# Kernel tuning notes

Measured on AMD Instinct MI355X. Metric: run time of the kernel, lower is better.

The kernel has to match this reference:

```python
import jax, jax.numpy as jnp
import numpy as np

B, N, H, M = 1, 1024, 64, 32


def _posenc(n, d):
    # sinusoidal positional encoding, matches torch PositionalEncoding (eval mode, no dropout)
    pos = jnp.arange(n, dtype=jnp.float32)[:, None]
    div = jnp.exp(jnp.arange(0, d, 2, dtype=jnp.float32) * (-np.log(10000.0) / d))
    ang = pos * div  # [n, d//2]
    pe = jnp.zeros((n, d), jnp.float32)
    pe = pe.at[:, 0::2].set(jnp.sin(ang))
    pe = pe.at[:, 1::2].set(jnp.cos(ang))
    return pe


def _egnn(x, h, m2f, w_msg, b_msg, w_pos, b_pos, w_feat, b_feat):
    # x: [B,N,3], h: [B,N,Hd], m2f: [B,N,N] float pair mask (diag zero)
    Bn, Nn, Hd = h.shape
    m2 = m2f[..., None]
    # r[b,i,j] = x[b,j] - x[b,i]  (torch: x.unsqueeze(-3) - x.unsqueeze(-2))
    r = (x[:, None, :, :] - x[:, :, None, :]) * m2  # [B,N,N,3]
    d2 = jnp.sum(r * r, axis=-1)  # [B,N,N]
    # message_mlp(cat(hi, hj, d2)): hi[b,i,j]=h[j], hj[b,i,j]=h[i]
    # split weight to avoid materializing the N x N x (2H+1) concat
    Wa, Wb, wd = w_msg[:, :Hd], w_msg[:, Hd:2 * Hd], w_msg[:, 2 * Hd]
    A = h @ Wa.T   # [B,N,M], contribution of h_j (hi slot)
    Bm = h @ Wb.T  # [B,N,M], contribution of h_i (hj slot)
    m = jax.nn.relu(A[:, None, :, :] + Bm[:, :, None, :] + d2[..., None] * wd + b_msg) * m2  # [B,N,N,M]
    mx = (m @ w_pos.T + b_pos) * r  # [B,N,N,3]
    x = x + jnp.sum(mx, axis=-2) / (Nn - 1)
    msum = jnp.sum(m, axis=-2)  # [B,N,M]
    h = jnp.concatenate([h, msum], axis=-1) @ w_feat.T + b_feat  # [B,N,Hd]
    return x, h


def setup_inputs() -> dict:
    key = jax.random.key(0)
    ks = jax.random.split(key, 16)
    def lin_w(k, o, i):
        return (jax.random.normal(k, (o, i), jnp.float32) / np.sqrt(i)).astype(jnp.float32)
    def lin_b(k, o):
        return (jax.random.normal(k, (o,), jnp.float32) * 0.02).astype(jnp.float32)
    return {
        'positions': jax.random.normal(ks[0], (B, N, 3), jnp.float32),
        'features': jax.random.normal(ks[1], (B, N, H), jnp.float32),
        'mask': jnp.ones((B, N), dtype=bool),
        'w_msg1': lin_w(ks[2], M, 2 * H + 1), 'b_msg1': lin_b(ks[3], M),
        'w_pos1': lin_w(ks[4], 3, M), 'b_pos1': lin_b(ks[5], 3),
        'w_feat1': lin_w(ks[6], H, M + H), 'b_feat1': lin_b(ks[7], H),
        'w_msg2': lin_w(ks[8], M, 2 * H + 1), 'b_msg2': lin_b(ks[9], M),
        'w_pos2': lin_w(ks[10], 3, M), 'b_pos2': lin_b(ks[11], 3),
        'w_feat2': lin_w(ks[12], H, M + H), 'b_feat2': lin_b(ks[13], H),
        't': 0,
    }


def reference(positions, features, mask,
              w_msg1, b_msg1, w_pos1, b_pos1, w_feat1, b_feat1,
              w_msg2, b_msg2, w_pos2, b_pos2, w_feat2, b_feat2, t):
    Bn, Nn, Hd = features.shape
    h = features + _posenc(Nn, Hd)[None]
    mask2 = mask[:, None, :] & mask[:, :, None]
    mask2 = mask2 & (~jnp.eye(Nn, dtype=bool))[None]  # zero self-pairs
    m2f = mask2.astype(positions.dtype)
    x = positions
    x, h = _egnn(x, h, m2f, w_msg1, b_msg1, w_pos1, b_pos1, w_feat1, b_feat1)
    h = jax.nn.relu(h)
    x, h = _egnn(x, h, m2f, w_msg2, b_msg2, w_pos2, b_pos2, w_feat2, b_feat2)
    return x
```

## Files before the change

kernel.cpp:

```cpp
#include <hip/hip_runtime.h>

#define N    1024
#define HD   64
#define MD   32
#define BLK  256
#define BLKP 512
#define WROW (2 * HD + 1)

__global__ __launch_bounds__(BLK) void k_p0(const float* __restrict__ feat,
                                            const float* __restrict__ wmsg,
                                            const float* __restrict__ bmsg,
                                            float* __restrict__ h0,
                                            float* __restrict__ A,
                                            float* __restrict__ Bb)
{
    __shared__ float scr[4160 + 4 * HD];
    const int tid = threadIdx.x;
    const int n0  = blockIdx.x * 4;

    for (int u = tid; u < MD * WROW; u += BLK) scr[u] = wmsg[u];
    float* hrow = scr + 4160;
    {
        const int n = n0 + (tid >> 6), d = tid & 63;
        const float div = expf((float)(d & ~1) * (-9.210340371976184f / 64.0f));
        const float ang = (float)n * div;
        const float pe  = (d & 1) ? cosf(ang) : sinf(ang);
        const float hv  = feat[n * HD + d] + pe;
        h0[n * HD + d] = hv;
        hrow[tid] = hv;
    }
    __syncthreads();
    if (tid < 4 * MD) {
        const int nl = tid >> 5, m = tid & 31;
        const float* wa = scr + m * WROW;
        const float* hr = hrow + nl * HD;
        float sa = 0.f, sb = bmsg[m];
#pragma unroll
        for (int c = 0; c < HD; c++) {
            const float hv = hr[c];
            sa = fmaf(hv, wa[c], sa);
            sb = fmaf(hv, wa[HD + c], sb);
        }
        const int n = n0 + nl;
        A[n * MD + m]  = sa;
        Bb[n * MD + m] = sb;
    }
}

template<int LAYER1>
__global__ __launch_bounds__(BLKP) void k_pair(
    const float* __restrict__ xsrc, const float* __restrict__ Aap,
    const float* __restrict__ Bbp, const float* __restrict__ wmsg,
    const float* __restrict__ wpos, const float* __restrict__ bpos,
    float* __restrict__ xout,
    const float* __restrict__ h0, const float* __restrict__ wf,
    const float* __restrict__ bf, const float* __restrict__ wmsg2,
    const float* __restrict__ bmsg2, float* __restrict__ A2,
    float* __restrict__ B2)
{
    const int tid   = threadIdx.x;
    const int wid   = tid >> 6;
    const int lane  = tid & 63;
    const int jslot = lane & 7;
    const int kq    = lane >> 3;

    __shared__ float4 rd[2 * N];
    __shared__ float  wacc[8][8];
    __shared__ float  msAl[8][MD];
    __shared__ float  msBl[8][MD];
    __shared__ float  SxL[3];
    __shared__ float  msF[2][MD];
    __shared__ float  h0r[2][HD];
    __shared__ float  h1r[2][HD];
    float4* rdA = rd;
    float4* rdB = rd + N;

    const int iA = blockIdx.x, iB = blockIdx.x + N / 2;
    const float xiA0 = xsrc[iA * 3 + 0], xiA1 = xsrc[iA * 3 + 1], xiA2 = xsrc[iA * 3 + 2];
    const float xiB0 = xsrc[iB * 3 + 0], xiB1 = xsrc[iB * 3 + 1], xiB2 = xsrc[iB * 3 + 2];

    float sx0 = 0.f, sx1 = 0.f, sx2 = 0.f;
#pragma unroll
    for (int q = 0; q < N / BLKP; q++) {
        const int j = q * BLKP + tid;
        const float xj0 = xsrc[j * 3 + 0];
        const float xj1 = xsrc[j * 3 + 1];
        const float xj2 = xsrc[j * 3 + 2];
        sx0 += xj0; sx1 += xj1; sx2 += xj2;
        float r0 = xj0 - xiA0, r1 = xj1 - xiA1, r2 = xj2 - xiA2;
        rdA[j] = make_float4(r0, r1, r2, fmaf(r0, r0, fmaf(r1, r1, r2 * r2)));
        r0 = xj0 - xiB0; r1 = xj1 - xiB1; r2 = xj2 - xiB2;
        rdB[j] = make_float4(r0, r1, r2, fmaf(r0, r0, fmaf(r1, r1, r2 * r2)));
    }
#pragma unroll
    for (int off = 32; off > 0; off >>= 1) {
        sx0 += __shfl_xor(sx0, off);
        sx1 += __shfl_xor(sx1, off);
        sx2 += __shfl_xor(sx2, off);
    }
    if (lane == 0) { wacc[wid][0] = sx0; wacc[wid][1] = sx1; wacc[wid][2] = sx2; }
    __syncthreads();
    if (tid == 0) {
        float s0 = 0.f, s1 = 0.f, s2 = 0.f;
#pragma unroll
        for (int w = 0; w < 8; w++) { s0 += wacc[w][0]; s1 += wacc[w][1]; s2 += wacc[w][2]; }
        SxL[0] = s0; SxL[1] = s1; SxL[2] = s2;
    }

    const float4 biA4 = *(const float4*)(Bbp + iA * MD + kq * 4);
    const float4 biB4 = *(const float4*)(Bbp + iB * MD + kq * 4);
    const float4 wpx4 = *(const float4*)(wpos + kq * 4);
    const float4 wpy4 = *(const float4*)(wpos + MD + kq * 4);
    const float4 wpz4 = *(const float4*)(wpos + 2 * MD + kq * 4);
    float wd4[4];
#pragma unroll
    for (int kk = 0; kk < 4; kk++) wd4[kk] = wmsg[(kq * 4 + kk) * WROW + 2 * HD];
    const float biA[4] = {biA4.x, biA4.y, biA4.z, biA4.w};
    const float biB[4] = {biB4.x, biB4.y, biB4.z, biB4.w};
    const float wpx[4] = {wpx4.x, wpx4.y, wpx4.z, wpx4.w};
    const float wpy[4] = {wpy4.x, wpy4.y, wpy4.z, wpy4.w};
    const float wpz[4] = {wpz4.x, wpz4.y, wpz4.z, wpz4.w};

    float PAx[4] = {0,0,0,0}, PAy[4] = {0,0,0,0}, PAz[4] = {0,0,0,0};
    float PBx[4] = {0,0,0,0}, PBy[4] = {0,0,0,0}, PBz[4] = {0,0,0,0};
    float msA[4] = {0,0,0,0}, msB[4] = {0,0,0,0};

    const int jb = wid * (N / 8);
#pragma unroll 8
    for (int it = 0; it < N / 8 / 8; it++) {
        const int j = jb + it * 8 + jslot;
        const float4 a4 = *(const float4*)(Aap + j * MD + kq * 4);
        const float4 fA = rdA[j];
        const float4 fB = rdB[j];
        const float av[4] = {a4.x, a4.y, a4.z, a4.w};
#pragma unroll
        for (int kk = 0; kk < 4; kk++) {
            const float mA = fmaxf(fmaf(fA.w, wd4[kk], av[kk] + biA[kk]), 0.f);
            const float mB = fmaxf(fmaf(fB.w, wd4[kk], av[kk] + biB[kk]), 0.f);
            if (LAYER1) { msA[kk] += mA; msB[kk] += mB; }
            PAx[kk] = fmaf(mA, fA.x, PAx[kk]);
            PAy[kk] = fmaf(mA, fA.y, PAy[kk]);
            PAz[kk] = fmaf(mA, fA.z, PAz[kk]);
            PBx[kk] = fmaf(mB, fB.x, PBx[kk]);
            PBy[kk] = fmaf(mB, fB.y, PBy[kk]);
            PBz[kk] = fmaf(mB, fB.z, PBz[kk]);
        }
    }

    float vA0 = 0.f, vA1 = 0.f, vA2 = 0.f, vB0 = 0.f, vB1 = 0.f, vB2 = 0.f;
#pragma unroll
    for (int kk = 0; kk < 4; kk++) {
        vA0 = fmaf(PAx[kk], wpx[kk], vA0);
        vA1 = fmaf(PAy[kk], wpy[kk], vA1);
        vA2 = fmaf(PAz[kk], wpz[kk], vA2);
        vB0 = fmaf(PBx[kk], wpx[kk], vB0);
        vB1 = fmaf(PBy[kk], wpy[kk], vB1);
        vB2 = fmaf(PBz[kk], wpz[kk], vB2);
    }
#pragma unroll
    for (int off = 32; off > 0; off >>= 1) {
        vA0 += __shfl_xor(vA0, off); vA1 += __shfl_xor(vA1, off); vA2 += __shfl_xor(vA2, off);
        vB0 += __shfl_xor(vB0, off); vB1 += __shfl_xor(vB1, off); vB2 += __shfl_xor(vB2, off);
    }
    if (LAYER1) {
#pragma unroll
        for (int off = 1; off <= 4; off <<= 1) {
#pragma unroll
            for (int kk = 0; kk < 4; kk++) {
                msA[kk] += __shfl_xor(msA[kk], off);
                msB[kk] += __shfl_xor(msB[kk], off);
            }
        }
    }
    __syncthreads();
    if (lane == 0) {
        wacc[wid][0] = vA0; wacc[wid][1] = vA1; wacc[wid][2] = vA2;
        wacc[wid][3] = vB0; wacc[wid][4] = vB1; wacc[wid][5] = vB2;
    }
    if (LAYER1 && jslot == 0) {
#pragma unroll
        for (int kk = 0; kk < 4; kk++) {
            msAl[wid][kq * 4 + kk] = msA[kk];
            msBl[wid][kq * 4 + kk] = msB[kk];
        }
    }
    __syncthreads();

    if (tid == 0) {
        const float bp0 = bpos[0], bp1 = bpos[1], bp2 = bpos[2];
        float aA0 = 0.f, aA1 = 0.f, aA2 = 0.f, aB0 = 0.f, aB1 = 0.f, aB2 = 0.f;
#pragma unroll
        for (int w = 0; w < 8; w++) {
            aA0 += wacc[w][0]; aA1 += wacc[w][1]; aA2 += wacc[w][2];
            aB0 += wacc[w][3]; aB1 += wacc[w][4]; aB2 += wacc[w][5];
        }
        const float inv = 1.0f / 1023.0f;
        xout[iA * 3 + 0] = xiA0 + (aA0 + bp0 * (SxL[0] - (float)N * xiA0)) * inv;
        xout[iA * 3 + 1] = xiA1 + (aA1 + bp1 * (SxL[1] - (float)N * xiA1)) * inv;
        xout[iA * 3 + 2] = xiA2 + (aA2 + bp2 * (SxL[2] - (float)N * xiA2)) * inv;
        xout[iB * 3 + 0] = xiB0 + (aB0 + bp0 * (SxL[0] - (float)N * xiB0)) * inv;
        xout[iB * 3 + 1] = xiB1 + (aB1 + bp1 * (SxL[1] - (float)N * xiB1)) * inv;
        xout[iB * 3 + 2] = xiB2 + (aB2 + bp2 * (SxL[2] - (float)N * xiB2)) * inv;
    }

    if (LAYER1) {
        float* scr = (float*)rd;
        if (tid < 2 * MD) {
            const int row = tid >> 5, k = tid & 31;
            const int i = row ? iB : iA;
            const float (*ml)[MD] = row ? msBl : msAl;
            float s = 0.f;
#pragma unroll
            for (int w = 0; w < 8; w++) s += ml[w][k];
            s -= fmaxf(Aap[i * MD + k] + Bbp[i * MD + k], 0.f);
            msF[row][k] = s;
        }
        for (int u = tid; u < HD * (HD + MD); u += BLKP) {
            const int o = u / (HD + MD), c = u - o * (HD + MD);
            scr[o * 97 + c] = wf[u];
        }
        if (tid < 2 * HD) {
            const int row = tid >> 6, d = tid & 63;
            h0r[row][d] = h0[(row ? iB : iA) * HD + d];
        }
        __syncthreads();
        if (tid < 2 * HD) {
            const int row = tid >> 6, o = tid & 63;
            const float* w = scr + o * 97;
            float s = bf[o];
#pragma unroll
            for (int c = 0; c < HD; c++) s = fmaf(h0r[row][c], w[c], s);
#pragma unroll
            for (int k = 0; k < MD; k++) s = fmaf(msF[row][k], w[HD + k], s);
            h1r[row][o] = fmaxf(s, 0.f);
        }
        __syncthreads();
        for (int u = tid; u < MD * WROW; u += BLKP) scr[u] = wmsg2[u];
        __syncthreads();
        if (tid < 2 * MD) {
            const int row = tid >> 5, m = tid & 31;
            const float* wa = scr + m * WROW;
            const float* hr = h1r[row];
            float sa = 0.f, sb = bmsg2[m];
#pragma unroll
            for (int c = 0; c < HD; c++) {
                const float hv = hr[c];
                sa = fmaf(hv, wa[c], sa);
                sb = fmaf(hv, wa[HD + c], sb);
            }
            const int i = row ? iB : iA;
            A2[i * MD + m] = sa;
            B2[i * MD + m] = sb;
        }
    }
}

extern "C" void kernel_launch(void* const* d_in, const int* in_sizes, int n_in,
                              void* d_out, int out_size, void* d_ws, size_t ws_size,
                              hipStream_t stream)
{
    const float* pos     = (const float*)d_in[0];
    const float* feat    = (const float*)d_in[1];
    const float* w_msg1  = (const float*)d_in[3];
    const float* b_msg1  = (const float*)d_in[4];
    const float* w_pos1  = (const float*)d_in[5];
    const float* b_pos1  = (const float*)d_in[6];
    const float* w_feat1 = (const float*)d_in[7];
    const float* b_feat1 = (const float*)d_in[8];
    const float* w_msg2  = (const float*)d_in[9];
    const float* b_msg2  = (const float*)d_in[10];
    const float* w_pos2  = (const float*)d_in[11];
    const float* b_pos2  = (const float*)d_in[12];

    float* ws  = (float*)d_ws;
    float* h0  = ws;
    float* A1  = h0  + N * HD;
    float* B1  = A1  + N * MD;
    float* x1  = B1  + N * MD;
    float* A2  = x1  + N * 4;
    float* B2  = A2  + N * MD;

    k_p0<<<N / 4, BLK, 0, stream>>>(feat, w_msg1, b_msg1, h0, A1, B1);
    k_pair<1><<<N / 2, BLKP, 0, stream>>>(pos, A1, B1, w_msg1, w_pos1, b_pos1, x1,
                                          h0, w_feat1, b_feat1, w_msg2, b_msg2, A2, B2);
    k_pair<0><<<N / 2, BLKP, 0, stream>>>(x1, A2, B2, w_msg2, w_pos2, b_pos2,
                                          (float*)d_out,
                                          nullptr, nullptr, nullptr, nullptr,
                                          nullptr, nullptr, nullptr);
}
```

Baseline: 39.74 us.

## Split pair kernel over j-halves with partial sums and separate finalize kernels

```diff
diff --git a/kernel.cpp b/kernel.cpp
--- a/kernel.cpp
+++ b/kernel.cpp
@@ -1,11 +1,13 @@
 #include <hip/hip_runtime.h>
 
 #define N    1024
+#define HALF 512
 #define HD   64
 #define MD   32
 #define BLK  256
 #define BLKP 512
 #define WROW (2 * HD + 1)
+#define PS   80
 
 __global__ __launch_bounds__(BLK) void k_p0(const float* __restrict__ feat,
                                             const float* __restrict__ wmsg,
@@ -47,16 +49,11 @@
     }
 }
 
-template<int LAYER1>
-__global__ __launch_bounds__(BLKP) void k_pair(
+template<int WRITE_MS>
+__global__ __launch_bounds__(BLKP) void k_pairp(
     const float* __restrict__ xsrc, const float* __restrict__ Aap,
     const float* __restrict__ Bbp, const float* __restrict__ wmsg,
-    const float* __restrict__ wpos, const float* __restrict__ bpos,
-    float* __restrict__ xout,
-    const float* __restrict__ h0, const float* __restrict__ wf,
-    const float* __restrict__ bf, const float* __restrict__ wmsg2,
-    const float* __restrict__ bmsg2, float* __restrict__ A2,
-    float* __restrict__ B2)
+    const float* __restrict__ wpos, float* __restrict__ part)
 {
     const int tid   = threadIdx.x;
     const int wid   = tid >> 6;
@@ -64,47 +61,38 @@
     const int jslot = lane & 7;
     const int kq    = lane >> 3;
 
-    __shared__ float4 rd[2 * N];
-    __shared__ float  wacc[8][8];
+    __shared__ float4 rdA[HALF];
+    __shared__ float4 rdB[HALF];
+    __shared__ float  sxacc[8][3];
+    __shared__ float  wacc[8][6];
     __shared__ float  msAl[8][MD];
     __shared__ float  msBl[8][MD];
-    __shared__ float  SxL[3];
-    __shared__ float  msF[2][MD];
-    __shared__ float  h0r[2][HD];
-    __shared__ float  h1r[2][HD];
-    float4* rdA = rd;
-    float4* rdB = rd + N;
-
-    const int iA = blockIdx.x, iB = blockIdx.x + N / 2;
+
+    const int bb   = blockIdx.x & (HALF - 1);
+    const int half = blockIdx.x >> 9;
+    const int iA = bb, iB = bb + HALF;
+    const int j0 = half * HALF;
+
     const float xiA0 = xsrc[iA * 3 + 0], xiA1 = xsrc[iA * 3 + 1], xiA2 = xsrc[iA * 3 + 2];
     const float xiB0 = xsrc[iB * 3 + 0], xiB1 = xsrc[iB * 3 + 1], xiB2 = xsrc[iB * 3 + 2];
 
-    float sx0 = 0.f, sx1 = 0.f, sx2 = 0.f;
-#pragma unroll
-    for (int q = 0; q < N / BLKP; q++) {
-        const int j = q * BLKP + tid;
+    {
+        const int j = j0 + tid;
         const float xj0 = xsrc[j * 3 + 0];
         const float xj1 = xsrc[j * 3 + 1];
         const float xj2 = xsrc[j * 3 + 2];
-        sx0 += xj0; sx1 += xj1; sx2 += xj2;
+        float sx0 = xj0, sx1 = xj1, sx2 = xj2;
         float r0 = xj0 - xiA0, r1 = xj1 - xiA1, r2 = xj2 - xiA2;
-        rdA[j] = make_float4(r0, r1, r2, fmaf(r0, r0, fmaf(r1, r1, r2 * r2)));
+        rdA[tid] = make_float4(r0, r1, r2, fmaf(r0, r0, fmaf(r1, r1, r2 * r2)));
         r0 = xj0 - xiB0; r1 = xj1 - xiB1; r2 = xj2 - xiB2;
-        rdB[j] = make_float4(r0, r1, r2, fmaf(r0, r0, fmaf(r1, r1, r2 * r2)));
-    }
-#pragma unroll
-    for (int off = 32; off > 0; off >>= 1) {
-        sx0 += __shfl_xor(sx0, off);
-        sx1 += __shfl_xor(sx1, off);
-        sx2 += __shfl_xor(sx2, off);
-    }
-    if (lane == 0) { wacc[wid][0] = sx0; wacc[wid][1] = sx1; wacc[wid][2] = sx2; }
-    __syncthreads();
-    if (tid == 0) {
-        float s0 = 0.f, s1 = 0.f, s2 = 0.f;
-#pragma unroll
-        for (int w = 0; w < 8; w++) { s0 += wacc[w][0]; s1 += wacc[w][1]; s2 += wacc[w][2]; }
-        SxL[0] = s0; SxL[1] = s1; SxL[2] = s2;
+        rdB[tid] = make_float4(r0, r1, r2, fmaf(r0, r0, fmaf(r1, r1, r2 * r2)));
+#pragma unroll
+        for (int off = 32; off > 0; off >>= 1) {
+            sx0 += __shfl_xor(sx0, off);
+            sx1 += __shfl_xor(sx1, off);
+            sx2 += __shfl_xor(sx2, off);
+        }
+        if (lane == 0) { sxacc[wid][0] = sx0; sxacc[wid][1] = sx1; sxacc[wid][2] = sx2; }
     }
 
     const float4 biA4 = *(const float4*)(Bbp + iA * MD + kq * 4);
@@ -125,19 +113,21 @@
     float PBx[4] = {0,0,0,0}, PBy[4] = {0,0,0,0}, PBz[4] = {0,0,0,0};
     float msA[4] = {0,0,0,0}, msB[4] = {0,0,0,0};
 
-    const int jb = wid * (N / 8);
+    __syncthreads();
+
+    const int jbl = wid * 64;
 #pragma unroll 8
-    for (int it = 0; it < N / 8 / 8; it++) {
-        const int j = jb + it * 8 + jslot;
-        const float4 a4 = *(const float4*)(Aap + j * MD + kq * 4);
-        const float4 fA = rdA[j];
-        const float4 fB = rdB[j];
+    for (int it = 0; it < 8; it++) {
+        const int jl = jbl + it * 8 + jslot;
+        const float4 a4 = *(const float4*)(Aap + (j0 + jl) * MD + kq * 4);
+        const float4 fA = rdA[jl];
+        const float4 fB = rdB[jl];
         const float av[4] = {a4.x, a4.y, a4.z, a4.w};
 #pragma unroll
         for (int kk = 0; kk < 4; kk++) {
             const float mA = fmaxf(fmaf(fA.w, wd4[kk], av[kk] + biA[kk]), 0.f);
             const float mB = fmaxf(fmaf(fB.w, wd4[kk], av[kk] + biB[kk]), 0.f);
-            if (LAYER1) { msA[kk] += mA; msB[kk] += mB; }
+            if (WRITE_MS) { msA[kk] += mA; msB[kk] += mB; }
             PAx[kk] = fmaf(mA, fA.x, PAx[kk]);
             PAy[kk] = fmaf(mA, fA.y, PAy[kk]);
             PAz[kk] = fmaf(mA, fA.z, PAz[kk]);
@@ -162,7 +152,7 @@
         vA0 += __shfl_xor(vA0, off); vA1 += __shfl_xor(vA1, off); vA2 += __shfl_xor(vA2, off);
         vB0 += __shfl_xor(vB0, off); vB1 += __shfl_xor(vB1, off); vB2 += __shfl_xor(vB2, off);
     }
-    if (LAYER1) {
+    if (WRITE_MS) {
 #pragma unroll
         for (int off = 1; off <= 4; off <<= 1) {
 #pragma unroll
@@ -172,12 +162,11 @@
             }
         }
     }
-    __syncthreads();
     if (lane == 0) {
         wacc[wid][0] = vA0; wacc[wid][1] = vA1; wacc[wid][2] = vA2;
         wacc[wid][3] = vB0; wacc[wid][4] = vB1; wacc[wid][5] = vB2;
     }
-    if (LAYER1 && jslot == 0) {
+    if (WRITE_MS && jslot == 0) {
 #pragma unroll
         for (int kk = 0; kk < 4; kk++) {
             msAl[wid][kq * 4 + kk] = msA[kk];
@@ -186,72 +175,122 @@
     }
     __syncthreads();
 
+    float* po = part + blockIdx.x * PS;
     if (tid == 0) {
-        const float bp0 = bpos[0], bp1 = bpos[1], bp2 = bpos[2];
-        float aA0 = 0.f, aA1 = 0.f, aA2 = 0.f, aB0 = 0.f, aB1 = 0.f, aB2 = 0.f;
-#pragma unroll
-        for (int w = 0; w < 8; w++) {
-            aA0 += wacc[w][0]; aA1 += wacc[w][1]; aA2 += wacc[w][2];
-            aB0 += wacc[w][3]; aB1 += wacc[w][4]; aB2 += wacc[w][5];
-        }
+#pragma unroll
+        for (int c = 0; c < 6; c++) {
+            float s = 0.f;
+#pragma unroll
+            for (int w = 0; w < 8; w++) s += wacc[w][c];
+            po[c] = s;
+        }
+#pragma unroll
+        for (int c = 0; c < 3; c++) {
+            float s = 0.f;
+#pragma unroll
+            for (int w = 0; w < 8; w++) s += sxacc[w][c];
+            po[6 + c] = s;
+        }
+    }
+    if (WRITE_MS && tid < 2 * MD) {
+        const int row = tid >> 5, k = tid & 31;
+        const float (*ml)[MD] = row ? msBl : msAl;
+        float s = 0.f;
+#pragma unroll
+        for (int w = 0; w < 8; w++) s += ml[w][k];
+        po[16 + row * 32 + k] = s;
+    }
+}
+
+__global__ __launch_bounds__(BLK) void k_fin1(
+    const float* __restrict__ xsrc, const float* __restrict__ part,
+    const float* __restrict__ Aap, const float* __restrict__ Bbp,
+    const float* __restrict__ bpos, const float* __restrict__ h0,
+    const float* __restrict__ wf, const float* __restrict__ bf,
+    const float* __restrict__ wmsg2, const float* __restrict__ bmsg2,
+    float* __restrict__ x1, float* __restrict__ A2, float* __restrict__ B2)
+{
+    __shared__ float scr[6208];
+    __shared__ float msF[2][MD], h0r[2][HD], h1r[2][HD];
+    const int tid = threadIdx.x;
+    const int bb  = blockIdx.x;
+    const int iA = bb, iB = bb + HALF;
+    const float* p0 = part + bb * PS;
+    const float* p1 = part + (bb + HALF) * PS;
+
+    if (tid < 2 * MD) {
+        const int row = tid >> 5, k = tid & 31;
+        const int i = row ? iB : iA;
+        float s = p0[16 + row * 32 + k] + p1[16 + row * 32 + k];
+        s -= fmaxf(Aap[i * MD + k] + Bbp[i * MD + k], 0.f);
+        msF[row][k] = s;
+    }
+    for (int u = tid; u < HD * (HD + MD); u += BLK) {
+        const int o = u / (HD + MD), c = u - o * (HD + MD);
+        scr[o * 97 + c] = wf[u];
+    }
+    if (tid < 2 * HD) {
+        const int row = tid >> 6, d = tid & 63;
+        h0r[row][d] = h0[(row ? iB : iA) * HD + d];
+    }
+    if (tid == 0) {
+        const float bp[3] = {bpos[0], bpos[1], bpos[2]};
         const float inv = 1.0f / 1023.0f;
-        xout[iA * 3 + 0] = xiA0 + (aA0 + bp0 * (SxL[0] - (float)N * xiA0)) * inv;
-        xout[iA * 3 + 1] = xiA1 + (aA1 + bp1 * (SxL[1] - (float)N * xiA1)) * inv;
-        xout[iA * 3 + 2] = xiA2 + (aA2 + bp2 * (SxL[2] - (float)N * xiA2)) * inv;
-        xout[iB * 3 + 0] = xiB0 + (aB0 + bp0 * (SxL[0] - (float)N * xiB0)) * inv;
-        xout[iB * 3 + 1] = xiB1 + (aB1 + bp1 * (SxL[1] - (float)N * xiB1)) * inv;
-        xout[iB * 3 + 2] = xiB2 + (aB2 + bp2 * (SxL[2] - (float)N * xiB2)) * inv;
-    }
-
-    if (LAYER1) {
-        float* scr = (float*)rd;
-        if (tid < 2 * MD) {
-            const int row = tid >> 5, k = tid & 31;
-            const int i = row ? iB : iA;
-            const float (*ml)[MD] = row ? msBl : msAl;
-            float s = 0.f;
-#pragma unroll
-            for (int w = 0; w < 8; w++) s += ml[w][k];
-            s -= fmaxf(Aap[i * MD + k] + Bbp[i * MD + k], 0.f);
-            msF[row][k] = s;
-        }
-        for (int u = tid; u < HD * (HD + MD); u += BLKP) {
-            const int o = u / (HD + MD), c = u - o * (HD + MD);
-            scr[o * 97 + c] = wf[u];
-        }
-        if (tid < 2 * HD) {
-            const int row = tid >> 6, d = tid & 63;
-            h0r[row][d] = h0[(row ? iB : iA) * HD + d];
-        }
-        __syncthreads();
-        if (tid < 2 * HD) {
-            const int row = tid >> 6, o = tid & 63;
-            const float* w = scr + o * 97;
-            float s = bf[o];
-#pragma unroll
-            for (int c = 0; c < HD; c++) s = fmaf(h0r[row][c], w[c], s);
-#pragma unroll
-            for (int k = 0; k < MD; k++) s = fmaf(msF[row][k], w[HD + k], s);
-            h1r[row][o] = fmaxf(s, 0.f);
-        }
-        __syncthreads();
-        for (int u = tid; u < MD * WROW; u += BLKP) scr[u] = wmsg2[u];
-        __syncthreads();
-        if (tid < 2 * MD) {
-            const int row = tid >> 5, m = tid & 31;
-            const float* wa = scr + m * WROW;
-            const float* hr = h1r[row];
-            float sa = 0.f, sb = bmsg2[m];
-#pragma unroll
-            for (int c = 0; c < HD; c++) {
-                const float hv = hr[c];
-                sa = fmaf(hv, wa[c], sa);
-                sb = fmaf(hv, wa[HD + c], sb);
-            }
-            const int i = row ? iB : iA;
-            A2[i * MD + m] = sa;
-            B2[i * MD + m] = sb;
-        }
+#pragma unroll
+        for (int c = 0; c < 3; c++) {
+            const float Sx = p0[6 + c] + p1[6 + c];
+            const float xa = xsrc[iA * 3 + c];
+            const float xb = xsrc[iB * 3 + c];
+            x1[iA * 3 + c] = xa + (p0[c] + p1[c] + bp[c] * (Sx - (float)N * xa)) * inv;
+            x1[iB * 3 + c] = xb + (p0[3 + c] + p1[3 + c] + bp[c] * (Sx - (float)N * xb)) * inv;
+        }
+    }
+    __syncthreads();
+    if (tid < 2 * HD) {
+        const int row = tid >> 6, o = tid & 63;
+        const float* w = scr + o * 97;
+        float s = bf[o];
+#pragma unroll
+        for (int c = 0; c < HD; c++) s = fmaf(h0r[row][c], w[c], s);
+#pragma unroll
+        for (int k = 0; k < MD; k++) s = fmaf(msF[row][k], w[HD + k], s);
+        h1r[row][o] = fmaxf(s, 0.f);
+    }
+    __syncthreads();
+    for (int u = tid; u < MD * WROW; u += BLK) scr[u] = wmsg2[u];
+    __syncthreads();
+    if (tid < 2 * MD) {
+        const int row = tid >> 5, m = tid & 31;
+        const float* wa = scr + m * WROW;
+        const float* hr = h1r[row];
+        float sa = 0.f, sb = bmsg2[m];
+#pragma unroll
+        for (int c = 0; c < HD; c++) {
+            const float hv = hr[c];
+            sa = fmaf(hv, wa[c], sa);
+            sb = fmaf(hv, wa[HD + c], sb);
+        }
+        const int i = row ? iB : iA;
+        A2[i * MD + m] = sa;
+        B2[i * MD + m] = sb;
+    }
+}
+
+__global__ __launch_bounds__(BLK) void k_fin2(
+    const float* __restrict__ xsrc, const float* __restrict__ part,
+    const float* __restrict__ bpos, float* __restrict__ out)
+{
+    const int i = blockIdx.x * BLK + threadIdx.x;
+    const int bb = i & (HALF - 1), row = i >> 9;
+    const float* p0 = part + bb * PS;
+    const float* p1 = part + (bb + HALF) * PS;
+    const float inv = 1.0f / 1023.0f;
+#pragma unroll
+    for (int c = 0; c < 3; c++) {
+        const float Sx = p0[6 + c] + p1[6 + c];
+        const float v  = p0[row * 3 + c] + p1[row * 3 + c];
+        const float xi = xsrc[i * 3 + c];
+        out[i * 3 + c] = xi + (v + bpos[c] * (Sx - (float)N * xi)) * inv;
     }
 }
 
@@ -272,19 +311,19 @@
     const float* w_pos2  = (const float*)d_in[11];
     const float* b_pos2  = (const float*)d_in[12];
 
-    float* ws  = (float*)d_ws;
-    float* h0  = ws;
-    float* A1  = h0  + N * HD;
-    float* B1  = A1  + N * MD;
-    float* x1  = B1  + N * MD;
-    float* A2  = x1  + N * 4;
-    float* B2  = A2  + N * MD;
+    float* ws   = (float*)d_ws;
+    float* h0   = ws;
+    float* A1   = h0  + N * HD;
+    float* B1   = A1  + N * MD;
+    float* x1   = B1  + N * MD;
+    float* A2   = x1  + N * 4;
+    float* B2   = A2  + N * MD;
+    float* part = B2  + N * MD;
 
     k_p0<<<N / 4, BLK, 0, stream>>>(feat, w_msg1, b_msg1, h0, A1, B1);
-    k_pair<1><<<N / 2, BLKP, 0, stream>>>(pos, A1, B1, w_msg1, w_pos1, b_pos1, x1,
-                                          h0, w_feat1, b_feat1, w_msg2, b_msg2, A2, B2);
-    k_pair<0><<<N / 2, BLKP, 0, stream>>>(x1, A2, B2, w_msg2, w_pos2, b_pos2,
-                                          (float*)d_out,
-                                          nullptr, nullptr, nullptr, nullptr,
-                                          nullptr, nullptr, nullptr);
-}
+    k_pairp<1><<<2 * HALF, BLKP, 0, stream>>>(pos, A1, B1, w_msg1, w_pos1, part);
+    k_fin1<<<HALF, BLK, 0, stream>>>(pos, part, A1, B1, b_pos1, h0,
+                                     w_feat1, b_feat1, w_msg2, b_msg2, x1, A2, B2);
+    k_pairp<0><<<2 * HALF, BLKP, 0, stream>>>(x1, A2, B2, w_msg2, w_pos2, part);
+    k_fin2<<<N / BLK, BLK, 0, stream>>>(x1, part, b_pos2, (float*)d_out);
+}
```

New measurement: 56.40 us. 1.42x slower.

## Compute pair messages in packed fp16 with fdot2 position projection

Applied to the files above, without the earlier changes.

```diff
diff --git a/kernel.cpp b/kernel.cpp
--- a/kernel.cpp
+++ b/kernel.cpp
@@ -7,12 +7,28 @@
 #define BLKP 512
 #define WROW (2 * HD + 1)
 
+typedef _Float16 h2 __attribute__((ext_vector_type(2)));
+
+__device__ __forceinline__ float dot2(h2 a, h2 b, float c)
+{
+#if __has_builtin(__builtin_amdgcn_fdot2)
+    return __builtin_amdgcn_fdot2(a, b, c, false);
+#else
+    return c + (float)a[0] * (float)b[0] + (float)a[1] * (float)b[1];
+#endif
+}
+__device__ __forceinline__ h2 pack2(float x, float y)
+{
+    h2 r; r[0] = (_Float16)x; r[1] = (_Float16)y; return r;
+}
+
 __global__ __launch_bounds__(BLK) void k_p0(const float* __restrict__ feat,
                                             const float* __restrict__ wmsg,
                                             const float* __restrict__ bmsg,
                                             float* __restrict__ h0,
                                             float* __restrict__ A,
-                                            float* __restrict__ Bb)
+                                            float* __restrict__ Bb,
+                                            _Float16* __restrict__ Ah)
 {
     __shared__ float scr[4160 + 4 * HD];
     const int tid = threadIdx.x;
@@ -44,19 +60,20 @@
         const int n = n0 + nl;
         A[n * MD + m]  = sa;
         Bb[n * MD + m] = sb;
+        Ah[n * MD + m] = (_Float16)sa;
     }
 }
 
 template<int LAYER1>
 __global__ __launch_bounds__(BLKP) void k_pair(
     const float* __restrict__ xsrc, const float* __restrict__ Aap,
-    const float* __restrict__ Bbp, const float* __restrict__ wmsg,
-    const float* __restrict__ wpos, const float* __restrict__ bpos,
-    float* __restrict__ xout,
+    const _Float16* __restrict__ Ahp, const float* __restrict__ Bbp,
+    const float* __restrict__ wmsg, const float* __restrict__ wpos,
+    const float* __restrict__ bpos, float* __restrict__ xout,
     const float* __restrict__ h0, const float* __restrict__ wf,
     const float* __restrict__ bf, const float* __restrict__ wmsg2,
     const float* __restrict__ bmsg2, float* __restrict__ A2,
-    float* __restrict__ B2)
+    float* __restrict__ B2, _Float16* __restrict__ A2h)
 {
     const int tid   = threadIdx.x;
     const int wid   = tid >> 6;
@@ -88,9 +105,11 @@
         const float xj2 = xsrc[j * 3 + 2];
         sx0 += xj0; sx1 += xj1; sx2 += xj2;
         float r0 = xj0 - xiA0, r1 = xj1 - xiA1, r2 = xj2 - xiA2;
-        rdA[j] = make_float4(r0, r1, r2, fmaf(r0, r0, fmaf(r1, r1, r2 * r2)));
+        float d2 = fmaf(r0, r0, fmaf(r1, r1, r2 * r2));
+        rdA[j] = make_float4(r0, r1, r2, __builtin_bit_cast(float, pack2(d2, d2)));
         r0 = xj0 - xiB0; r1 = xj1 - xiB1; r2 = xj2 - xiB2;
-        rdB[j] = make_float4(r0, r1, r2, fmaf(r0, r0, fmaf(r1, r1, r2 * r2)));
+        d2 = fmaf(r0, r0, fmaf(r1, r1, r2 * r2));
+        rdB[j] = make_float4(r0, r1, r2, __builtin_bit_cast(float, pack2(d2, d2)));
     }
 #pragma unroll
     for (int off = 32; off > 0; off >>= 1) {
@@ -112,95 +131,101 @@
     const float4 wpx4 = *(const float4*)(wpos + kq * 4);
     const float4 wpy4 = *(const float4*)(wpos + MD + kq * 4);
     const float4 wpz4 = *(const float4*)(wpos + 2 * MD + kq * 4);
-    float wd4[4];
-#pragma unroll
-    for (int kk = 0; kk < 4; kk++) wd4[kk] = wmsg[(kq * 4 + kk) * WROW + 2 * HD];
-    const float biA[4] = {biA4.x, biA4.y, biA4.z, biA4.w};
-    const float biB[4] = {biB4.x, biB4.y, biB4.z, biB4.w};
-    const float wpx[4] = {wpx4.x, wpx4.y, wpx4.z, wpx4.w};
-    const float wpy[4] = {wpy4.x, wpy4.y, wpy4.z, wpy4.w};
-    const float wpz[4] = {wpz4.x, wpz4.y, wpz4.z, wpz4.w};
-
-    float PAx[4] = {0,0,0,0}, PAy[4] = {0,0,0,0}, PAz[4] = {0,0,0,0};
-    float PBx[4] = {0,0,0,0}, PBy[4] = {0,0,0,0}, PBz[4] = {0,0,0,0};
-    float msA[4] = {0,0,0,0}, msB[4] = {0,0,0,0};
+    const h2 biA01 = pack2(biA4.x, biA4.y), biA23 = pack2(biA4.z, biA4.w);
+    const h2 biB01 = pack2(biB4.x, biB4.y), biB23 = pack2(biB4.z, biB4.w);
+    const h2 wpx01 = pack2(wpx4.x, wpx4.y), wpx23 = pack2(wpx4.z, wpx4.w);
+    const h2 wpy01 = pack2(wpy4.x, wpy4.y), wpy23 = pack2(wpy4.z, wpy4.w);
+    const h2 wpz01 = pack2(wpz4.x, wpz4.y), wpz23 = pack2(wpz4.z, wpz4.w);
+    const h2 wd01 = pack2(wmsg[(kq * 4 + 0) * WROW + 2 * HD],
+                          wmsg[(kq * 4 + 1) * WROW + 2 * HD]);
+    const h2 wd23 = pack2(wmsg[(kq * 4 + 2) * WROW + 2 * HD],
+                          wmsg[(kq * 4 + 3) * WROW + 2 * HD]);
+    const h2 hz = pack2(0.f, 0.f);
+
+    float aA0 = 0.f, aA1 = 0.f, aA2 = 0.f, aB0 = 0.f, aB1 = 0.f, aB2 = 0.f;
+    h2 msA01 = hz, msA23 = hz, msB01 = hz, msB23 = hz;
 
     const int jb = wid * (N / 8);
 #pragma unroll 8
     for (int it = 0; it < N / 8 / 8; it++) {
         const int j = jb + it * 8 + jslot;
-        const float4 a4 = *(const float4*)(Aap + j * MD + kq * 4);
+        const uint2 au = *(const uint2*)(Ahp + j * MD + kq * 4);
+        const h2 a01 = __builtin_bit_cast(h2, au.x);
+        const h2 a23 = __builtin_bit_cast(h2, au.y);
         const float4 fA = rdA[j];
         const float4 fB = rdB[j];
-        const float av[4] = {a4.x, a4.y, a4.z, a4.w};
-#pragma unroll
-        for (int kk = 0; kk < 4; kk++) {
-            const float mA = fmaxf(fmaf(fA.w, wd4[kk], av[kk] + biA[kk]), 0.f);
-            const float mB = fmaxf(fmaf(fB.w, wd4[kk], av[kk] + biB[kk]), 0.f);
-            if (LAYER1) { msA[kk] += mA; msB[kk] += mB; }
-            PAx[kk] = fmaf(mA, fA.x, PAx[kk]);
-            PAy[kk] = fmaf(mA, fA.y, PAy[kk]);
-            PAz[kk] = fmaf(mA, fA.z, PAz[kk]);
-            PBx[kk] = fmaf(mB, fB.x, PBx[kk]);
-            PBy[kk] = fmaf(mB, fB.y, PBy[kk]);
-            PBz[kk] = fmaf(mB, fB.z, PBz[kk]);
-        }
-    }
-
-    float vA0 = 0.f, vA1 = 0.f, vA2 = 0.f, vB0 = 0.f, vB1 = 0.f, vB2 = 0.f;
-#pragma unroll
-    for (int kk = 0; kk < 4; kk++) {
-        vA0 = fmaf(PAx[kk], wpx[kk], vA0);
-        vA1 = fmaf(PAy[kk], wpy[kk], vA1);
-        vA2 = fmaf(PAz[kk], wpz[kk], vA2);
-        vB0 = fmaf(PBx[kk], wpx[kk], vB0);
-        vB1 = fmaf(PBy[kk], wpy[kk], vB1);
-        vB2 = fmaf(PBz[kk], wpz[kk], vB2);
-    }
+        const h2 d2A = __builtin_bit_cast(h2, fA.w);
+        const h2 d2B = __builtin_bit_cast(h2, fB.w);
+
+        const h2 mA01 = __builtin_elementwise_max(d2A * wd01 + (a01 + biA01), hz);
+        const h2 mA23 = __builtin_elementwise_max(d2A * wd23 + (a23 + biA23), hz);
+        const h2 mB01 = __builtin_elementwise_max(d2B * wd01 + (a01 + biB01), hz);
+        const h2 mB23 = __builtin_elementwise_max(d2B * wd23 + (a23 + biB23), hz);
+        if (LAYER1) { msA01 += mA01; msA23 += mA23; msB01 += mB01; msB23 += mB23; }
+
+        const float sAx = dot2(mA23, wpx23, dot2(mA01, wpx01, 0.f));
+        const float sAy = dot2(mA23, wpy23, dot2(mA01, wpy01, 0.f));
+        const float sAz = dot2(mA23, wpz23, dot2(mA01, wpz01, 0.f));
+        const float sBx = dot2(mB23, wpx23, dot2(mB01, wpx01, 0.f));
+        const float sBy = dot2(mB23, wpy23, dot2(mB01, wpy01, 0.f));
+        const float sBz = dot2(mB23, wpz23, dot2(mB01, wpz01, 0.f));
+        aA0 = fmaf(sAx, fA.x, aA0);
+        aA1 = fmaf(sAy, fA.y, aA1);
+        aA2 = fmaf(sAz, fA.z, aA2);
+        aB0 = fmaf(sBx, fB.x, aB0);
+        aB1 = fmaf(sBy, fB.y, aB1);
+        aB2 = fmaf(sBz, fB.z, aB2);
+    }
+
 #pragma unroll
     for (int off = 32; off > 0; off >>= 1) {
-        vA0 += __shfl_xor(vA0, off); vA1 += __shfl_xor(vA1, off); vA2 += __shfl_xor(vA2, off);
-        vB0 += __shfl_xor(vB0, off); vB1 += __shfl_xor(vB1, off); vB2 += __shfl_xor(vB2, off);
-    }
+        aA0 += __shfl_xor(aA0, off); aA1 += __shfl_xor(aA1, off); aA2 += __shfl_xor(aA2, off);
+        aB0 += __shfl_xor(aB0, off); aB1 += __shfl_xor(aB1, off); aB2 += __shfl_xor(aB2, off);
+    }
+    float msAf[4], msBf[4];
     if (LAYER1) {
+        msAf[0] = (float)msA01[0]; msAf[1] = (float)msA01[1];
+        msAf[2] = (float)msA23[0]; msAf[3] = (float)msA23[1];
+        msBf[0] = (float)msB01[0]; msBf[1] = (float)msB01[1];
+        msBf[2] = (float)msB23[0]; msBf[3] = (float)msB23[1];
 #pragma unroll
         for (int off = 1; off <= 4; off <<= 1) {
 #pragma unroll
             for (int kk = 0; kk < 4; kk++) {
-                msA[kk] += __shfl_xor(msA[kk], off);
-                msB[kk] += __shfl_xor(msB[kk], off);
+                msAf[kk] += __shfl_xor(msAf[kk], off);
+                msBf[kk] += __shfl_xor(msBf[kk], off);
             }
         }
     }
     __syncthreads();
     if (lane == 0) {
-        wacc[wid][0] = vA0; wacc[wid][1] = vA1; wacc[wid][2] = vA2;
-        wacc[wid][3] = vB0; wacc[wid][4] = vB1; wacc[wid][5] = vB2;
+        wacc[wid][0] = aA0; wacc[wid][1] = aA1; wacc[wid][2] = aA2;
+        wacc[wid][3] = aB0; wacc[wid][4] = aB1; wacc[wid][5] = aB2;
     }
     if (LAYER1 && jslot == 0) {
 #pragma unroll
         for (int kk = 0; kk < 4; kk++) {
-            msAl[wid][kq * 4 + kk] = msA[kk];
-            msBl[wid][kq * 4 + kk] = msB[kk];
+            msAl[wid][kq * 4 + kk] = msAf[kk];
+            msBl[wid][kq * 4 + kk] = msBf[kk];
         }
     }
     __syncthreads();
 
     if (tid == 0) {
         const float bp0 = bpos[0], bp1 = bpos[1], bp2 = bpos[2];
-        float aA0 = 0.f, aA1 = 0.f, aA2 = 0.f, aB0 = 0.f, aB1 = 0.f, aB2 = 0.f;
+        float vA0 = 0.f, vA1 = 0.f, vA2 = 0.f, vB0 = 0.f, vB1 = 0.f, vB2 = 0.f;
 #pragma unroll
         for (int w = 0; w < 8; w++) {
-            aA0 += wacc[w][0]; aA1 += wacc[w][1]; aA2 += wacc[w][2];
-            aB0 += wacc[w][3]; aB1 += wacc[w][4]; aB2 += wacc[w][5];
+            vA0 += wacc[w][0]; vA1 += wacc[w][1]; vA2 += wacc[w][2];
+            vB0 += wacc[w][3]; vB1 += wacc[w][4]; vB2 += wacc[w][5];
         }
         const float inv = 1.0f / 1023.0f;
-        xout[iA * 3 + 0] = xiA0 + (aA0 + bp0 * (SxL[0] - (float)N * xiA0)) * inv;
-        xout[iA * 3 + 1] = xiA1 + (aA1 + bp1 * (SxL[1] - (float)N * xiA1)) * inv;
-        xout[iA * 3 + 2] = xiA2 + (aA2 + bp2 * (SxL[2] - (float)N * xiA2)) * inv;
-        xout[iB * 3 + 0] = xiB0 + (aB0 + bp0 * (SxL[0] - (float)N * xiB0)) * inv;
-        xout[iB * 3 + 1] = xiB1 + (aB1 + bp1 * (SxL[1] - (float)N * xiB1)) * inv;
-        xout[iB * 3 + 2] = xiB2 + (aB2 + bp2 * (SxL[2] - (float)N * xiB2)) * inv;
+        xout[iA * 3 + 0] = xiA0 + (vA0 + bp0 * (SxL[0] - (float)N * xiA0)) * inv;
+        xout[iA * 3 + 1] = xiA1 + (vA1 + bp1 * (SxL[1] - (float)N * xiA1)) * inv;
+        xout[iA * 3 + 2] = xiA2 + (vA2 + bp2 * (SxL[2] - (float)N * xiA2)) * inv;
+        xout[iB * 3 + 0] = xiB0 + (vB0 + bp0 * (SxL[0] - (float)N * xiB0)) * inv;
+        xout[iB * 3 + 1] = xiB1 + (vB1 + bp1 * (SxL[1] - (float)N * xiB1)) * inv;
+        xout[iB * 3 + 2] = xiB2 + (vB2 + bp2 * (SxL[2] - (float)N * xiB2)) * inv;
     }
 
     if (LAYER1) {
@@ -249,8 +274,9 @@
                 sb = fmaf(hv, wa[HD + c], sb);
             }
             const int i = row ? iB : iA;
-            A2[i * MD + m] = sa;
-            B2[i * MD + m] = sb;
+            A2[i * MD + m]  = sa;
+            B2[i * MD + m]  = sb;
+            A2h[i * MD + m] = (_Float16)sa;
         }
     }
 }
@@ -279,12 +305,15 @@
     float* x1  = B1  + N * MD;
     float* A2  = x1  + N * 4;
     float* B2  = A2  + N * MD;
-
-    k_p0<<<N / 4, BLK, 0, stream>>>(feat, w_msg1, b_msg1, h0, A1, B1);
-    k_pair<1><<<N / 2, BLKP, 0, stream>>>(pos, A1, B1, w_msg1, w_pos1, b_pos1, x1,
-                                          h0, w_feat1, b_feat1, w_msg2, b_msg2, A2, B2);
-    k_pair<0><<<N / 2, BLKP, 0, stream>>>(x1, A2, B2, w_msg2, w_pos2, b_pos2,
+    _Float16* Ah1 = (_Float16*)(B2 + N * MD);
+    _Float16* Ah2 = Ah1 + N * MD;
+
+    k_p0<<<N / 4, BLK, 0, stream>>>(feat, w_msg1, b_msg1, h0, A1, B1, Ah1);
+    k_pair<1><<<N / 2, BLKP, 0, stream>>>(pos, A1, Ah1, B1, w_msg1, w_pos1, b_pos1, x1,
+                                          h0, w_feat1, b_feat1, w_msg2, b_msg2,
+                                          A2, B2, Ah2);
+    k_pair<0><<<N / 2, BLKP, 0, stream>>>(x1, A2, Ah2, B2, w_msg2, w_pos2, b_pos2,
                                           (float*)d_out,
                                           nullptr, nullptr, nullptr, nullptr,
-                                          nullptr, nullptr, nullptr);
-}
+                                          nullptr, nullptr, nullptr, nullptr);
+}
```

New measurement: 36.00 us. 9.4% less time.
